# Optimization experiments

Measured on AMD Instinct MI355X. Metric: run time of the kernel, lower is better.

## Reference

```python
import jax, jax.numpy as jnp
import numpy as np

def setup_inputs() -> dict:
    key = jax.random.key(0)
    k1, k2, k3, k4 = jax.random.split(key, 4)
    B, T, D = 4, 4096, 256
    # xavier_normal_ with gain 0.002: std = 0.002 * sqrt(2/(D+D))
    std = 0.002 * np.sqrt(2.0 / (D + D))
    return {
        "x": jax.random.normal(k1, (B, T, D), dtype=jnp.float32),
        "W_k": jax.random.normal(k2, (D, D), dtype=jnp.float32) * std,
        "W_q": jax.random.normal(k3, (D, D), dtype=jnp.float32) * std,
        "W_v": jax.random.normal(k4, (D, D), dtype=jnp.float32) * std,
    }

def reference(x, W_k, W_q, W_v):
    # Projections: (B,T,D) @ (D,D) -> (B,T,D)
    K = jnp.einsum('btd,dk->btk', x, W_k)
    Q = jnp.einsum('btd,dq->btq', x, W_q)
    V = jnp.einsum('btd,dv->btv', x, W_v)
    # Note: original code has NO 1/sqrt(D) scaling.
    scores = jnp.einsum('bqd,bkd->bqk', Q, K)  # (B,T,T)
    attn = jax.nn.softmax(scores, axis=2)
    return jnp.einsum('bta,bav->btv', attn, V)
```

## Files before the change

### kernel.cpp

```cpp
#include <hip/hip_runtime.h>

typedef __attribute__((ext_vector_type(4))) float f32x4;
typedef __attribute__((ext_vector_type(8))) __bf16 bf16x8;
typedef __attribute__((ext_vector_type(4))) unsigned short u16x4;
typedef unsigned short u16;
typedef unsigned int u32;
typedef unsigned long long u64;

#define AS1 __attribute__((address_space(1)))
#define AS3 __attribute__((address_space(3)))

__device__ __forceinline__ void gload_lds16(const void* g, void* l) {
  __builtin_amdgcn_global_load_lds((const AS1 u32*)g, (AS3 u32*)l, 16, 0, 0);
}

__global__ __launch_bounds__(256) void k_flag(float* __restrict__ out, int n) {
  for (int i = blockIdx.x * 256 + threadIdx.x; i < n; i += gridDim.x * 256)
    out[i] = 1.0f;
}

__global__ __launch_bounds__(256) void k_cvt_x(const float* __restrict__ x,
                                               __bf16* __restrict__ xb) {
  int i = blockIdx.x * 256 + threadIdx.x;
  const f32x4* p = (const f32x4*)x;
  f32x4 a = p[i * 2], b = p[i * 2 + 1];
  bf16x8 o;
  o[0] = (__bf16)a[0]; o[1] = (__bf16)a[1]; o[2] = (__bf16)a[2]; o[3] = (__bf16)a[3];
  o[4] = (__bf16)b[0]; o[5] = (__bf16)b[1]; o[6] = (__bf16)b[2]; o[7] = (__bf16)b[3];
  ((bf16x8*)xb)[i] = o;
}

__global__ __launch_bounds__(256) void k_cvt_w(const float* __restrict__ Wk,
                                               const float* __restrict__ Wq,
                                               const float* __restrict__ Wv,
                                               __bf16* __restrict__ Wt) {
  const float* W = blockIdx.y == 0 ? Wk : (blockIdx.y == 1 ? Wq : Wv);
  int i = blockIdx.x * 256 + threadIdx.x;
  int n = i >> 8, k = i & 255;
  Wt[blockIdx.y * 65536 + i] = (__bf16)W[k * 256 + n];
}

__global__ __launch_bounds__(256) void k_proj(const __bf16* __restrict__ xb,
                                              const __bf16* __restrict__ Wt,
                                              __bf16* __restrict__ Kb,
                                              __bf16* __restrict__ Qb,
                                              __bf16* __restrict__ Vt) {
  __shared__ __bf16 As[128 * 64];
  __shared__ __bf16 Bs[128 * 64];
  int tid = threadIdx.x;
  int lane = tid & 63, w = tid >> 6;
  int l15 = lane & 15, l4 = lane >> 4;
  int m0 = blockIdx.x * 128, n0 = blockIdx.y * 128;
  int z = blockIdx.z;
  const __bf16* Wz = Wt + z * 65536;
  int wm = (w & 1) * 64, wn = (w >> 1) * 64;
  f32x4 acc[4][4];
  for (int a = 0; a < 4; ++a)
    for (int b = 0; b < 4; ++b) acc[a][b] = (f32x4){0.f, 0.f, 0.f, 0.f};

  for (int k0 = 0; k0 < 256; k0 += 64) {
    __syncthreads();
    for (int it = 0; it < 4; ++it) {
      int id = it * 256 + tid;
      int r = id >> 3, c = id & 7, sc = c ^ (r & 7);
      gload_lds16(xb + (u64)(m0 + r) * 256 + k0 + sc * 8, (char*)As + id * 16);
    }
    for (int it = 0; it < 4; ++it) {
      int id = it * 256 + tid;
      int r = id >> 3, c = id & 7, sc = c ^ (r & 7);
      gload_lds16(Wz + (u64)(n0 + r) * 256 + k0 + sc * 8, (char*)Bs + id * 16);
    }
    asm volatile("s_waitcnt vmcnt(0)" ::: "memory");
    __syncthreads();
    for (int ks = 0; ks < 2; ++ks) {
      bf16x8 af[4], bg[4];
      for (int mf = 0; mf < 4; ++mf) {
        int m = wm + mf * 16 + l15;
        int ch = (ks * 4 + l4) ^ (m & 7);
        af[mf] = *(const bf16x8*)((const char*)As + m * 128 + ch * 16);
      }
      for (int nf = 0; nf < 4; ++nf) {
        int n = wn + nf * 16 + l15;
        int ch = (ks * 4 + l4) ^ (n & 7);
        bg[nf] = *(const bf16x8*)((const char*)Bs + n * 128 + ch * 16);
      }
      for (int mf = 0; mf < 4; ++mf)
        for (int nf = 0; nf < 4; ++nf)
          acc[mf][nf] = __builtin_amdgcn_mfma_f32_16x16x32_bf16(af[mf], bg[nf],
                                                                acc[mf][nf], 0, 0, 0);
    }
  }
  if (z != 2) {
    __bf16* C = z == 0 ? Kb : Qb;
    for (int mf = 0; mf < 4; ++mf)
      for (int nf = 0; nf < 4; ++nf)
        for (int r = 0; r < 4; ++r) {
          int m = m0 + wm + mf * 16 + l4 * 4 + r;
          int n = n0 + wn + nf * 16 + l15;
          C[(u64)m * 256 + n] = (__bf16)acc[mf][nf][r];
        }
  } else {
    int bb = m0 >> 12;
    for (int mf = 0; mf < 4; ++mf)
      for (int nf = 0; nf < 4; ++nf) {
        int n = n0 + wn + nf * 16 + l15;
        int tb = (m0 & 4095) + wm + mf * 16 + l4 * 4;
        u16x4 pk;
        for (int r = 0; r < 4; ++r) {
          __bf16 h = (__bf16)acc[mf][nf][r];
          pk[r] = __builtin_bit_cast(u16, h);
        }
        *(u16x4*)(Vt + (u64)bb * 1048576 + (u64)n * 4096 + tb) = pk;
      }
  }
}

#define KVB 32
__global__ __launch_bounds__(256) void k_attn(const __bf16* __restrict__ Qb,
                                              const __bf16* __restrict__ Kb,
                                              const __bf16* __restrict__ Vt,
                                              float* __restrict__ Out) {
  extern __shared__ char smem[];
  __bf16* Ks0 = (__bf16*)smem;
  __bf16* Ks1 = (__bf16*)(smem + 16384);
  __bf16* Vs0 = (__bf16*)(smem + 32768);
  __bf16* Vs1 = (__bf16*)(smem + 49152);
  __bf16* Ps  = (__bf16*)(smem + 65536);
  float*  Ls  = (float*)(smem + 67584);
  int tid = threadIdx.x, lane = tid & 63, w = tid >> 6;
  int l15 = lane & 15, l4 = lane >> 4;
  int s = w & 1, h = w >> 1;
  int id8 = blockIdx.x & 7, slot = blockIdx.x >> 3;
  int b = id8 >> 1;
  int q0 = (((id8 & 1) << 6) | slot) << 5;
  const __bf16* Kbb = Kb + (u64)b * 4096 * 256;
  const __bf16* Vtb = Vt + (u64)b * 1048576;

  const __bf16* Qrow = Qb + (u64)(b * 4096 + q0 + s * 16 + l15) * 256;
  bf16x8 qf[8];
  for (int ks = 0; ks < 8; ++ks) qf[ks] = *(const bf16x8*)(Qrow + ks * 32 + l4 * 8);

  f32x4 oacc[2][4];
  for (int a = 0; a < 2; ++a)
    for (int c = 0; c < 4; ++c) oacc[a][c] = (f32x4){0.f, 0.f, 0.f, 0.f};
  float lp[4] = {0.f, 0.f, 0.f, 0.f};

  auto stageK = [&](int kv0, __bf16* dst) {
    for (int it = 0; it < 4; ++it) {
      int id = it * 256 + tid;
      int r = id >> 5, c = id & 31, sc = c ^ (r & 7);
      gload_lds16(Kbb + (u64)(kv0 + r) * 256 + sc * 8, (char*)dst + id * 16);
    }
  };
  auto stageV = [&](int kv0, __bf16* dst) {
    for (int it = 0; it < 4; ++it) {
      int id = it * 256 + tid;
      int d = id >> 2, c = id & 3, sc = c ^ (d & 3);
      gload_lds16(Vtb + (u64)d * 4096 + kv0 + sc * 8, (char*)dst + id * 16);
    }
  };

  stageK(0, Ks0);
  stageV(0, Vs0);
  asm volatile("s_waitcnt vmcnt(0)" ::: "memory");
  __syncthreads();

  for (int t = 0; t < 128; ++t) {
    __bf16* Kc = (t & 1) ? Ks1 : Ks0;
    __bf16* Vc = (t & 1) ? Vs1 : Vs0;
    __bf16* Kn = (t & 1) ? Ks0 : Ks1;
    __bf16* Vn = (t & 1) ? Vs0 : Vs1;
    if (t < 127) { stageK((t + 1) * KVB, Kn); stageV((t + 1) * KVB, Vn); }

    int kr = h * 16 + l15;
    f32x4 sa = (f32x4){0.f, 0.f, 0.f, 0.f}, sb = sa;
    for (int ks = 0; ks < 8; ks += 2) {
      int ch0 = (ks * 4 + l4) ^ (kr & 7);
      int ch1 = ((ks + 1) * 4 + l4) ^ (kr & 7);
      bf16x8 kf0 = *(const bf16x8*)((const char*)Kc + kr * 512 + ch0 * 16);
      bf16x8 kf1 = *(const bf16x8*)((const char*)Kc + kr * 512 + ch1 * 16);
      sa = __builtin_amdgcn_mfma_f32_16x16x32_bf16(qf[ks], kf0, sa, 0, 0, 0);
      sb = __builtin_amdgcn_mfma_f32_16x16x32_bf16(qf[ks + 1], kf1, sb, 0, 0, 0);
    }
    f32x4 sv = sa + sb;

    for (int r = 0; r < 4; ++r) {
      float p = __expf(sv[r]);
      lp[r] += p;
      int row = s * 16 + l4 * 4 + r;
      int ch = h * 2 + (l15 >> 3);
      int sc = ch ^ (row & 3);
      Ps[row * 32 + sc * 8 + (l15 & 7)] = (__bf16)p;
    }
    asm volatile("s_waitcnt lgkmcnt(0)\n\ts_barrier" ::: "memory");

    bf16x8 vf[4];
    for (int nf = 0; nf < 4; ++nf) {
      int d = w * 64 + nf * 16 + l15;
      int vc = l4 ^ (d & 3);
      vf[nf] = *(const bf16x8*)((const char*)Vc + d * 64 + vc * 16);
    }
    for (int mf = 0; mf < 2; ++mf) {
      int qr = mf * 16 + l15;
      int pc = l4 ^ (qr & 3);
      bf16x8 pa = *(const bf16x8*)(Ps + qr * 32 + pc * 8);
      for (int nf = 0; nf < 4; ++nf)
        oacc[mf][nf] = __builtin_amdgcn_mfma_f32_16x16x32_bf16(pa, vf[nf], oacc[mf][nf], 0, 0, 0);
    }
    asm volatile("s_waitcnt vmcnt(0) lgkmcnt(0)\n\ts_barrier" ::: "memory");
  }

  for (int m = 1; m < 16; m <<= 1)
    for (int r = 0; r < 4; ++r) lp[r] += __shfl_xor(lp[r], m, 64);
  if (l15 == 0)
    for (int r = 0; r < 4; ++r) Ls[h * 32 + s * 16 + l4 * 4 + r] = lp[r];
  __syncthreads();

  float* Ob = Out + (u64)(b * 4096 + q0) * 256;
  for (int mf = 0; mf < 2; ++mf)
    for (int r = 0; r < 4; ++r) {
      int row = mf * 16 + l4 * 4 + r;
      float inv = 1.0f / (Ls[row] + Ls[32 + row]);
      for (int nf = 0; nf < 4; ++nf)
        Ob[(u64)row * 256 + w * 64 + nf * 16 + l15] = oacc[mf][nf][r] * inv;
    }
}

extern "C" void kernel_launch(void* const* d_in, const int* in_sizes, int n_in,
                              void* d_out, int out_size, void* d_ws, size_t ws_size,
                              hipStream_t stream) {
  const float* x  = (const float*)d_in[0];
  const float* Wk = (const float*)d_in[1];
  const float* Wq = (const float*)d_in[2];
  const float* Wv = (const float*)d_in[3];
  float* out = (float*)d_out;
  char* ws = (char*)d_ws;

  const size_t NEEDED = 25559040;
  if (ws_size < NEEDED) {
    k_flag<<<1024, 256, 0, stream>>>(out, out_size);
    return;
  }
  __bf16* Wt = (__bf16*)ws;
  __bf16* Kb = (__bf16*)(ws + 393216);
  __bf16* Qb = (__bf16*)(ws + 8781824);
  __bf16* Vt = (__bf16*)(ws + 17170432);
  __bf16* xb = (__bf16*)d_out;

  k_cvt_x<<<2048, 256, 0, stream>>>(x, xb);
  k_cvt_w<<<dim3(256, 3), 256, 0, stream>>>(Wk, Wq, Wv, Wt);
  k_proj<<<dim3(128, 2, 3), 256, 0, stream>>>(xb, Wt, Kb, Qb, Vt);
  k_attn<<<512, 256, 67840, stream>>>(Qb, Kb, Vt, out);
}
```

Before: 233.9 us.

## Double attention query tile to 64 rows and merge conversion kernels

The attention kernel now processes 64 query rows per block instead of 32. Each wave computes two 16-row score fragments against the same K fragments and accumulates four output row fragments. This halves the K/V tile reloads per query and halves the grid to 256 blocks, which may underfill the GPU's compute units and raises register pressure. The x and weight bf16 conversion kernels are also fused into a single launch to save one kernel launch.

```diff
diff --git a/kernel.cpp b/kernel.cpp
--- a/kernel.cpp
+++ b/kernel.cpp
@@ -19,25 +19,28 @@
     out[i] = 1.0f;
 }
 
-__global__ __launch_bounds__(256) void k_cvt_x(const float* __restrict__ x,
-                                               __bf16* __restrict__ xb) {
-  int i = blockIdx.x * 256 + threadIdx.x;
-  const f32x4* p = (const f32x4*)x;
-  f32x4 a = p[i * 2], b = p[i * 2 + 1];
-  bf16x8 o;
-  o[0] = (__bf16)a[0]; o[1] = (__bf16)a[1]; o[2] = (__bf16)a[2]; o[3] = (__bf16)a[3];
-  o[4] = (__bf16)b[0]; o[5] = (__bf16)b[1]; o[6] = (__bf16)b[2]; o[7] = (__bf16)b[3];
-  ((bf16x8*)xb)[i] = o;
-}
-
-__global__ __launch_bounds__(256) void k_cvt_w(const float* __restrict__ Wk,
-                                               const float* __restrict__ Wq,
-                                               const float* __restrict__ Wv,
-                                               __bf16* __restrict__ Wt) {
-  const float* W = blockIdx.y == 0 ? Wk : (blockIdx.y == 1 ? Wq : Wv);
-  int i = blockIdx.x * 256 + threadIdx.x;
-  int n = i >> 8, k = i & 255;
-  Wt[blockIdx.y * 65536 + i] = (__bf16)W[k * 256 + n];
+__global__ __launch_bounds__(256) void k_cvt(const float* __restrict__ x,
+                                             const float* __restrict__ Wk,
+                                             const float* __restrict__ Wq,
+                                             const float* __restrict__ Wv,
+                                             __bf16* __restrict__ xb,
+                                             __bf16* __restrict__ Wt) {
+  int bx = blockIdx.x;
+  if (bx < 2048) {
+    int i = bx * 256 + threadIdx.x;
+    const f32x4* p = (const f32x4*)x;
+    f32x4 a = p[i * 2], b = p[i * 2 + 1];
+    bf16x8 o;
+    o[0] = (__bf16)a[0]; o[1] = (__bf16)a[1]; o[2] = (__bf16)a[2]; o[3] = (__bf16)a[3];
+    o[4] = (__bf16)b[0]; o[5] = (__bf16)b[1]; o[6] = (__bf16)b[2]; o[7] = (__bf16)b[3];
+    ((bf16x8*)xb)[i] = o;
+  } else {
+    int z = (bx - 2048) >> 8;
+    const float* W = z == 0 ? Wk : (z == 1 ? Wq : Wv);
+    int i = ((bx - 2048) & 255) * 256 + threadIdx.x;
+    int n = i >> 8, k = i & 255;
+    Wt[z * 65536 + i] = (__bf16)W[k * 256 + n];
+  }
 }
 
 __global__ __launch_bounds__(256) void k_proj(const __bf16* __restrict__ xb,
@@ -107,8 +110,8 @@
         int tb = (m0 & 4095) + wm + mf * 16 + l4 * 4;
         u16x4 pk;
         for (int r = 0; r < 4; ++r) {
-          __bf16 h = (__bf16)acc[mf][nf][r];
-          pk[r] = __builtin_bit_cast(u16, h);
+          __bf16 hh = (__bf16)acc[mf][nf][r];
+          pk[r] = __builtin_bit_cast(u16, hh);
         }
         *(u16x4*)(Vt + (u64)bb * 1048576 + (u64)n * 4096 + tb) = pk;
       }
@@ -126,24 +129,26 @@
   __bf16* Vs0 = (__bf16*)(smem + 32768);
   __bf16* Vs1 = (__bf16*)(smem + 49152);
   __bf16* Ps  = (__bf16*)(smem + 65536);
-  float*  Ls  = (float*)(smem + 67584);
+  float*  Ls  = (float*)(smem + 69632);
   int tid = threadIdx.x, lane = tid & 63, w = tid >> 6;
   int l15 = lane & 15, l4 = lane >> 4;
   int s = w & 1, h = w >> 1;
   int id8 = blockIdx.x & 7, slot = blockIdx.x >> 3;
   int b = id8 >> 1;
-  int q0 = (((id8 & 1) << 6) | slot) << 5;
+  int q0 = (((id8 & 1) << 5) | slot) << 6;
   const __bf16* Kbb = Kb + (u64)b * 4096 * 256;
   const __bf16* Vtb = Vt + (u64)b * 1048576;
 
-  const __bf16* Qrow = Qb + (u64)(b * 4096 + q0 + s * 16 + l15) * 256;
-  bf16x8 qf[8];
-  for (int ks = 0; ks < 8; ++ks) qf[ks] = *(const bf16x8*)(Qrow + ks * 32 + l4 * 8);
-
-  f32x4 oacc[2][4];
-  for (int a = 0; a < 2; ++a)
+  bf16x8 qf[2][8];
+  for (int mf = 0; mf < 2; ++mf) {
+    const __bf16* Qrow = Qb + (u64)(b * 4096 + q0 + s * 32 + mf * 16 + l15) * 256;
+    for (int ks = 0; ks < 8; ++ks) qf[mf][ks] = *(const bf16x8*)(Qrow + ks * 32 + l4 * 8);
+  }
+
+  f32x4 oacc[4][4];
+  for (int a = 0; a < 4; ++a)
     for (int c = 0; c < 4; ++c) oacc[a][c] = (f32x4){0.f, 0.f, 0.f, 0.f};
-  float lp[4] = {0.f, 0.f, 0.f, 0.f};
+  float lp[2][4] = {{0.f, 0.f, 0.f, 0.f}, {0.f, 0.f, 0.f, 0.f}};
 
   auto stageK = [&](int kv0, __bf16* dst) {
     for (int it = 0; it < 4; ++it) {
@@ -173,25 +178,27 @@
     if (t < 127) { stageK((t + 1) * KVB, Kn); stageV((t + 1) * KVB, Vn); }
 
     int kr = h * 16 + l15;
-    f32x4 sa = (f32x4){0.f, 0.f, 0.f, 0.f}, sb = sa;
+    f32x4 sa0 = (f32x4){0.f, 0.f, 0.f, 0.f}, sa1 = sa0, sb0 = sa0, sb1 = sa0;
     for (int ks = 0; ks < 8; ks += 2) {
       int ch0 = (ks * 4 + l4) ^ (kr & 7);
       int ch1 = ((ks + 1) * 4 + l4) ^ (kr & 7);
       bf16x8 kf0 = *(const bf16x8*)((const char*)Kc + kr * 512 + ch0 * 16);
       bf16x8 kf1 = *(const bf16x8*)((const char*)Kc + kr * 512 + ch1 * 16);
-      sa = __builtin_amdgcn_mfma_f32_16x16x32_bf16(qf[ks], kf0, sa, 0, 0, 0);
-      sb = __builtin_amdgcn_mfma_f32_16x16x32_bf16(qf[ks + 1], kf1, sb, 0, 0, 0);
-    }
-    f32x4 sv = sa + sb;
-
-    for (int r = 0; r < 4; ++r) {
-      float p = __expf(sv[r]);
-      lp[r] += p;
-      int row = s * 16 + l4 * 4 + r;
-      int ch = h * 2 + (l15 >> 3);
-      int sc = ch ^ (row & 3);
-      Ps[row * 32 + sc * 8 + (l15 & 7)] = (__bf16)p;
-    }
+      sa0 = __builtin_amdgcn_mfma_f32_16x16x32_bf16(qf[0][ks], kf0, sa0, 0, 0, 0);
+      sa1 = __builtin_amdgcn_mfma_f32_16x16x32_bf16(qf[1][ks], kf0, sa1, 0, 0, 0);
+      sb0 = __builtin_amdgcn_mfma_f32_16x16x32_bf16(qf[0][ks + 1], kf1, sb0, 0, 0, 0);
+      sb1 = __builtin_amdgcn_mfma_f32_16x16x32_bf16(qf[1][ks + 1], kf1, sb1, 0, 0, 0);
+    }
+    f32x4 sv[2] = {sa0 + sb0, sa1 + sb1};
+
+    for (int mf = 0; mf < 2; ++mf)
+      for (int r = 0; r < 4; ++r) {
+        float p = __expf(sv[mf][r]);
+        lp[mf][r] += p;
+        int row = s * 32 + mf * 16 + l4 * 4 + r;
+        int cs = (h * 2 + (l15 >> 3)) ^ l4;
+        Ps[row * 32 + cs * 8 + (l15 & 7)] = (__bf16)p;
+      }
     asm volatile("s_waitcnt lgkmcnt(0)\n\ts_barrier" ::: "memory");
 
     bf16x8 vf[4];
@@ -200,10 +207,10 @@
       int vc = l4 ^ (d & 3);
       vf[nf] = *(const bf16x8*)((const char*)Vc + d * 64 + vc * 16);
     }
-    for (int mf = 0; mf < 2; ++mf) {
+    for (int mf = 0; mf < 4; ++mf) {
       int qr = mf * 16 + l15;
-      int pc = l4 ^ (qr & 3);
-      bf16x8 pa = *(const bf16x8*)(Ps + qr * 32 + pc * 8);
+      int ch = l4 ^ ((l15 >> 2) & 3);
+      bf16x8 pa = *(const bf16x8*)(Ps + qr * 32 + ch * 8);
       for (int nf = 0; nf < 4; ++nf)
         oacc[mf][nf] = __builtin_amdgcn_mfma_f32_16x16x32_bf16(pa, vf[nf], oacc[mf][nf], 0, 0, 0);
     }
@@ -211,16 +218,19 @@
   }
 
   for (int m = 1; m < 16; m <<= 1)
-    for (int r = 0; r < 4; ++r) lp[r] += __shfl_xor(lp[r], m, 64);
+    for (int mf = 0; mf < 2; ++mf)
+      for (int r = 0; r < 4; ++r) lp[mf][r] += __shfl_xor(lp[mf][r], m, 64);
   if (l15 == 0)
-    for (int r = 0; r < 4; ++r) Ls[h * 32 + s * 16 + l4 * 4 + r] = lp[r];
+    for (int mf = 0; mf < 2; ++mf)
+      for (int r = 0; r < 4; ++r)
+        Ls[h * 64 + s * 32 + mf * 16 + l4 * 4 + r] = lp[mf][r];
   __syncthreads();
 
   float* Ob = Out + (u64)(b * 4096 + q0) * 256;
-  for (int mf = 0; mf < 2; ++mf)
+  for (int mf = 0; mf < 4; ++mf)
     for (int r = 0; r < 4; ++r) {
       int row = mf * 16 + l4 * 4 + r;
-      float inv = 1.0f / (Ls[row] + Ls[32 + row]);
+      float inv = 1.0f / (Ls[row] + Ls[64 + row]);
       for (int nf = 0; nf < 4; ++nf)
         Ob[(u64)row * 256 + w * 64 + nf * 16 + l15] = oacc[mf][nf][r] * inv;
     }
@@ -247,8 +257,7 @@
   __bf16* Vt = (__bf16*)(ws + 17170432);
   __bf16* xb = (__bf16*)d_out;
 
-  k_cvt_x<<<2048, 256, 0, stream>>>(x, xb);
-  k_cvt_w<<<dim3(256, 3), 256, 0, stream>>>(Wk, Wq, Wv, Wt);
+  k_cvt<<<2816, 256, 0, stream>>>(x, Wk, Wq, Wv, xb, Wt);
   k_proj<<<dim3(128, 2, 3), 256, 0, stream>>>(xb, Wt, Kb, Qb, Vt);
-  k_attn<<<512, 256, 67840, stream>>>(Qb, Kb, Vt, out);
-}
+  k_attn<<<256, 256, 70144, stream>>>(Qb, Kb, Vt, out);
+}
```

Result: faster. 214.4 us (-8.3%).
